# Kernel tuning notes

Hardware: AMD Instinct MI355X
Metric: run time of the kernel (lower is better)

Reference implementation:

```python
import jax, jax.numpy as jnp
import numpy as np

# ---- model hyperparameters (match init_kwargs) ----
D_MODEL = 1024
D_STATE = 128
EXPAND = 2
HEADDIM = 64
NGROUPS = 1
D_INNER = EXPAND * D_MODEL            # 2048
NHEADS = D_INNER // HEADDIM           # 32
ROPE_FRAC = 0.5
SPLIT = int(D_STATE * ROPE_FRAC)      # 64 rotary dims
NANG = SPLIT // 2                     # 32 rope angles
A_FLOOR = 1e-4
EPS = 1e-5
BATCH, SEQLEN = 1, 1024
SIZES = [D_INNER, D_INNER, D_STATE * NGROUPS, D_STATE * NGROUPS, NHEADS, NHEADS, NHEADS, NANG]
D_IN_PROJ = int(np.sum(SIZES))        # 4480


def setup_inputs() -> dict:
    key = jax.random.key(0)
    ks = jax.random.split(key, 6)
    u = jax.random.normal(ks[0], (BATCH, SEQLEN, D_MODEL), dtype=jnp.float32)
    W_in = jax.random.normal(ks[1], (D_MODEL, D_IN_PROJ), dtype=jnp.float32) * 0.02
    # dt_bias ~ log(dt) for dt in [1e-3, 0.1] -> around -4
    dt_bias = jax.random.normal(ks[2], (NHEADS,), dtype=jnp.float32) * 0.5 - 4.0
    B_bias = jnp.ones((NHEADS, D_STATE), jnp.float32) + 0.01 * jax.random.normal(ks[3], (NHEADS, D_STATE), dtype=jnp.float32)
    C_bias = jnp.ones((NHEADS, D_STATE), jnp.float32) + 0.01 * jax.random.normal(ks[4], (NHEADS, D_STATE), dtype=jnp.float32)
    Bn_w = jnp.ones((D_STATE,), jnp.float32)
    Cn_w = jnp.ones((D_STATE,), jnp.float32)
    D_param = jnp.ones((NHEADS,), jnp.float32)
    W_out = jax.random.normal(ks[5], (D_INNER, D_MODEL), dtype=jnp.float32) * 0.02
    return {"u": u, "W_in": W_in, "dt_bias": dt_bias, "B_bias": B_bias, "C_bias": C_bias,
            "Bn_w": Bn_w, "Cn_w": Cn_w, "D_param": D_param, "W_out": W_out}


def _rmsnorm(v, w):
    return v * jax.lax.rsqrt(jnp.mean(v * v, axis=-1, keepdims=True) + EPS) * w


def _forward(u, W_in, dt_bias, B_bias, C_bias, Bn_w, Cn_w, D_param, W_out):
    b, l, _ = u.shape
    proj = u @ W_in                                   # (b, l, d_in_proj)
    idx = np.cumsum(SIZES)[:-1]
    z, x, Bp, Cp, dd_dt, dd_A, trap_raw, ang = jnp.split(proj, idx, axis=-1)
    z = z.reshape(b, l, NHEADS, HEADDIM)
    x = x.reshape(b, l, NHEADS, HEADDIM)
    # A = clamp(-softplus(.), max=-A_floor);  dt = softplus(. + dt_bias)
    A = jnp.minimum(-jax.nn.softplus(dd_A), -A_FLOOR)          # (b,l,H)
    dt = jax.nn.softplus(dd_dt + dt_bias)                      # (b,l,H)
    a = jnp.exp(A * dt)                                        # decay per step
    lam = jax.nn.sigmoid(trap_raw)                             # trapezoid gate
    # RMSNorm on B/C (ngroups=1), then per-head additive bias
    Bn = _rmsnorm(Bp, Bn_w)                                    # (b,l,N)
    Cn = _rmsnorm(Cp, Cn_w)
    Bh = Bn[:, :, None, :] + B_bias                            # (b,l,H,N)
    Ch = Cn[:, :, None, :] + C_bias
    # data-dependent rotary: cumulative angle = cumsum(angles * dt)
    theta = jnp.cumsum(ang[:, :, None, :] * dt[..., None], axis=1)  # (b,l,H,NANG)
    cos, sin = jnp.cos(theta), jnp.sin(theta)

    def rope(v):
        d1, d2, rest = v[..., :NANG], v[..., NANG:SPLIT], v[..., SPLIT:]
        return jnp.concatenate([d1 * cos - d2 * sin, d1 * sin + d2 * cos, rest], axis=-1)

    Bh, Ch = rope(Bh), rope(Ch)

    tfirst = lambda v: jnp.moveaxis(v, 1, 0)
    inputs = (tfirst(Bh), tfirst(Ch), tfirst(x), tfirst(a), tfirst(dt), tfirst(lam))
    h0 = jnp.zeros((b, NHEADS, HEADDIM, D_STATE), jnp.float32)
    k0 = jnp.zeros((b, NHEADS, D_STATE), jnp.float32)
    v0 = jnp.zeros((b, NHEADS, HEADDIM), jnp.float32)

    def step(carry, inp):
        h, kp, vp = carry
        Bt, Ct, xt, at, dtt, lamt = inp
        # trapezoidal selective-scan update:
        # h_t = a_t h_{t-1} + dt_t (lam_t B_t x_t + (1-lam_t) a_t B_{t-1} x_{t-1})
        cur = jnp.einsum('bhp,bhn->bhpn', xt, Bt) * (dtt * lamt)[..., None, None]
        prv = jnp.einsum('bhp,bhn->bhpn', vp, kp) * (dtt * (1.0 - lamt) * at)[..., None, None]
        h = at[..., None, None] * h + cur + prv
        yt = jnp.einsum('bhn,bhpn->bhp', Ct, h)
        return (h, Bt, xt), yt

    _, y = jax.lax.scan(step, (h0, k0, v0), inputs)          # (l,b,H,P)
    y = jnp.moveaxis(y, 0, 1) + D_param[None, None, :, None] * x
    y = y * jax.nn.silu(z)                                    # gated output (no out-proj norm)
    return y.reshape(b, l, D_INNER) @ W_out


def reference(u, W_in, dt_bias, B_bias, C_bias, Bn_w, Cn_w, D_param, W_out):
    return _forward(u, W_in, dt_bias, B_bias, C_bias, Bn_w, Cn_w, D_param, W_out)
```

## Files before the change

### kernel.cpp

```cpp
#include <hip/hip_runtime.h>
#include <stdint.h>

#define SEQ     1024
#define DPROJ   4480

typedef __attribute__((ext_vector_type(8))) short short8;
typedef __attribute__((ext_vector_type(4))) float f4;

__device__ __forceinline__ short f2b(float f){
  union { float f; uint32_t u; } v; v.f = f;
  uint32_t r = (v.u + 0x7fffu + ((v.u >> 16) & 1u)) >> 16;
  return (short)(uint16_t)r;
}
__device__ __forceinline__ float b2f(uint16_t u){
  union { uint32_t u; float f; } v; v.u = ((uint32_t)u) << 16; return v.f;
}
__device__ __forceinline__ uint32_t pack2(float lo, float hi){
  return (uint32_t)(uint16_t)f2b(lo) | ((uint32_t)(uint16_t)f2b(hi) << 16);
}
__device__ __forceinline__ float softplus_f(float x){
  return x > 20.f ? x : log1pf(__expf(x));
}
__device__ __forceinline__ void gload_lds16(const short* g, short* l){
  __builtin_amdgcn_global_load_lds((const __attribute__((address_space(1))) void*)g,
                                   (__attribute__((address_space(3))) void*)l, 16, 0, 0);
}

__global__ __launch_bounds__(256) void cast_kernel(const float* __restrict__ in, short* __restrict__ out){
  int i = (blockIdx.x * 256 + threadIdx.x) * 4;
  f4 v = *(const f4*)(in + i);
  uint2 pk; pk.x = pack2(v.x, v.y); pk.y = pack2(v.z, v.w);
  *(uint2*)(out + i) = pk;
}

__global__ __launch_bounds__(256) void transpose_cast(const float* __restrict__ in, short* __restrict__ out,
                                                      int R, int C, int lda, int c0){
  __shared__ float tile[32][132];
  int bc = blockIdx.x * 32;
  int br = blockIdx.y * 128;
  int tid = threadIdx.x;
  int c = tid & 31, r0 = tid >> 5;
  #pragma unroll
  for (int i = 0; i < 16; i++){
    int r = r0 + i * 8;
    tile[c][r] = in[(size_t)(br + r) * lda + c0 + bc + c];
  }
  __syncthreads();
  #pragma unroll
  for (int i = 0; i < 4; i++){
    int task = tid + 256 * i;
    int cc = task >> 5;
    int rg = (task & 31) * 4;
    f4 v = *(const f4*)&tile[cc][rg];
    uint2 pk; pk.x = pack2(v.x, v.y); pk.y = pack2(v.z, v.w);
    *(uint2*)(out + (size_t)(bc + cc) * R + br + rg) = pk;
  }
}

__global__ __launch_bounds__(256) void gemm1_kernel(const short* __restrict__ A, const short* __restrict__ Bt,
                                                    float* __restrict__ C){
  const int M = 1024, N = 4480, K = 1024;
  __shared__ __align__(16) short As[128 * 32];
  __shared__ __align__(16) short Bs[160 * 32];
  const int tid  = threadIdx.x;
  const int wave = tid >> 6;
  const int lane = tid & 63;
  const int m0 = blockIdx.y * 128;
  const int n0 = blockIdx.x * 160;
  const int wm = (wave >> 1) * 64;
  const int wn = (wave & 1) * 80;
  const int quad = lane >> 4;
  const int r16  = lane & 15;

  f4 acc[4][5];
  #pragma unroll
  for (int i = 0; i < 4; i++)
    #pragma unroll
    for (int j = 0; j < 5; j++) acc[i][j] = (f4){0.f, 0.f, 0.f, 0.f};

  const int row0 = tid >> 2;
  const int kq   = tid & 3;
  const short* gA0 = A  + (size_t)(m0 + row0) * K + kq * 8;
  const short* gA1 = A  + (size_t)(m0 + row0 + 64) * K + kq * 8;
  const short* gB0 = Bt + (size_t)(n0 + row0) * K + kq * 8;
  const short* gB1 = Bt + (size_t)(n0 + row0 + 64) * K + kq * 8;
  const short* gB2 = Bt + (size_t)(n0 + row0 + 128) * K + kq * 8;
  short* lA0 = &As[(size_t)tid * 8];
  short* lA1 = &As[(size_t)(tid + 256) * 8];
  short* lB0 = &Bs[(size_t)tid * 8];
  short* lB1 = &Bs[(size_t)(tid + 256) * 8];
  short* lB2 = &Bs[(size_t)(tid + 512) * 8];

  for (int kt = 0; kt < 32; ++kt){
    const int ko = kt * 32;
    __syncthreads();
    gload_lds16(gA0 + ko, lA0);
    gload_lds16(gA1 + ko, lA1);
    gload_lds16(gB0 + ko, lB0);
    gload_lds16(gB1 + ko, lB1);
    if (tid < 128) gload_lds16(gB2 + ko, lB2);
    __syncthreads();
    short8 af[4], bf[5];
    #pragma unroll
    for (int i = 0; i < 4; i++)
      af[i] = *(const short8*)&As[(wm + i * 16 + r16) * 32 + quad * 8];
    #pragma unroll
    for (int j = 0; j < 5; j++)
      bf[j] = *(const short8*)&Bs[(wn + j * 16 + r16) * 32 + quad * 8];
    #pragma unroll
    for (int i = 0; i < 4; i++)
      #pragma unroll
      for (int j = 0; j < 5; j++)
        acc[i][j] = __builtin_amdgcn_mfma_f32_16x16x32_bf16(af[i], bf[j], acc[i][j], 0, 0, 0);
  }

  #pragma unroll
  for (int i = 0; i < 4; i++)
    #pragma unroll
    for (int j = 0; j < 5; j++)
      #pragma unroll
      for (int rr = 0; rr < 4; ++rr){
        int row = m0 + wm + i * 16 + quad * 4 + rr;
        int col = n0 + wn + j * 16 + r16;
        C[(size_t)row * N + col] = acc[i][j][rr];
      }
}

__global__ __launch_bounds__(256) void gemm2_kernel(const short* __restrict__ A, const short* __restrict__ Bt,
                                                    float* __restrict__ C){
  const int N = 1024, K = 2048, klen = 512;
  __shared__ __align__(16) short As[128 * 32];
  __shared__ __align__(16) short Bs[128 * 32];
  const int tid  = threadIdx.x;
  const int wave = tid >> 6;
  const int lane = tid & 63;
  const int m0 = blockIdx.y * 128;
  const int n0 = blockIdx.x * 128;
  const int k0 = blockIdx.z * klen;
  const int wm = (wave >> 1) * 64;
  const int wn = (wave & 1) * 64;
  const int quad = lane >> 4;
  const int r16  = lane & 15;

  f4 acc[4][4];
  #pragma unroll
  for (int i = 0; i < 4; i++)
    #pragma unroll
    for (int j = 0; j < 4; j++) acc[i][j] = (f4){0.f, 0.f, 0.f, 0.f};

  const int row0 = tid >> 2;
  const int kq   = tid & 3;
  const short* gA0 = A  + (size_t)(m0 + row0) * K + k0 + kq * 8;
  const short* gA1 = A  + (size_t)(m0 + row0 + 64) * K + k0 + kq * 8;
  const short* gB0 = Bt + (size_t)(n0 + row0) * K + k0 + kq * 8;
  const short* gB1 = Bt + (size_t)(n0 + row0 + 64) * K + k0 + kq * 8;
  short* lA0 = &As[(size_t)tid * 8];
  short* lA1 = &As[(size_t)(tid + 256) * 8];
  short* lB0 = &Bs[(size_t)tid * 8];
  short* lB1 = &Bs[(size_t)(tid + 256) * 8];

  for (int kt = 0; kt < klen / 32; ++kt){
    const int ko = kt * 32;
    __syncthreads();
    gload_lds16(gA0 + ko, lA0);
    gload_lds16(gA1 + ko, lA1);
    gload_lds16(gB0 + ko, lB0);
    gload_lds16(gB1 + ko, lB1);
    __syncthreads();
    short8 af[4], bf[4];
    #pragma unroll
    for (int i = 0; i < 4; i++){
      af[i] = *(const short8*)&As[(wm + i * 16 + r16) * 32 + quad * 8];
      bf[i] = *(const short8*)&Bs[(wn + i * 16 + r16) * 32 + quad * 8];
    }
    #pragma unroll
    for (int i = 0; i < 4; i++)
      #pragma unroll
      for (int j = 0; j < 4; j++)
        acc[i][j] = __builtin_amdgcn_mfma_f32_16x16x32_bf16(af[i], bf[j], acc[i][j], 0, 0, 0);
  }

  #pragma unroll
  for (int i = 0; i < 4; i++)
    #pragma unroll
    for (int j = 0; j < 4; j++)
      #pragma unroll
      for (int rr = 0; rr < 4; ++rr){
        int row = m0 + wm + i * 16 + quad * 4 + rr;
        int col = n0 + wn + j * 16 + r16;
        unsafeAtomicAdd(&C[(size_t)row * N + col], acc[i][j][rr]);
      }
}

__global__ __launch_bounds__(256) void scanL_kernel(const float* __restrict__ proj,
                                                    const float* __restrict__ dt_bias,
                                                    float* __restrict__ Lcum, float* __restrict__ u2b,
                                                    float* __restrict__ c1b, float* __restrict__ dtb){
  int h = blockIdx.x;
  int tid = threadIdx.x;
  int t0 = tid * 4;
  float dtbias = dt_bias[h];
  float dt5[5], lam5[5];
  #pragma unroll
  for (int i = 0; i < 5; i++){
    int t = t0 + i;
    if (t < 1024){
      const float* row = proj + (size_t)t * DPROJ;
      dt5[i]  = softplus_f(row[4352 + h] + dtbias);
      lam5[i] = 1.f / (1.f + __expf(-row[4416 + h]));
    } else { dt5[i] = 0.f; lam5[i] = 0.f; }
  }
  float v[4], c1[4], c2n[4];
  #pragma unroll
  for (int i = 0; i < 4; i++){
    int t = t0 + i;
    const float* row = proj + (size_t)t * DPROJ;
    float Ah = -fmaxf(softplus_f(row[4384 + h]), 1e-4f);
    v[i]   = Ah * dt5[i];
    c1[i]  = dt5[i] * lam5[i];
    c2n[i] = dt5[i + 1] * (1.f - lam5[i + 1]);
  }
  v[1] += v[0]; v[2] += v[1]; v[3] += v[2];
  float tot = v[3], sc = tot;
  int lane = tid & 63, wave = tid >> 6;
  #pragma unroll
  for (int off = 1; off < 64; off <<= 1){
    float n = __shfl_up(sc, off, 64);
    if (lane >= off) sc += n;
  }
  __shared__ float wsum[4];
  if (lane == 63) wsum[wave] = sc;
  __syncthreads();
  float base = sc - tot;
  for (int w = 0; w < wave; ++w) base += wsum[w];
  #pragma unroll
  for (int i = 0; i < 4; i++){
    int t = t0 + i;
    Lcum[h * 1024 + t] = base + v[i];
    u2b[h * 1024 + t]  = c1[i] + c2n[i];
    c1b[h * 1024 + t]  = c1[i];
    dtb[h * 1024 + t]  = dt5[i];
  }
}

__global__ __launch_bounds__(256) void theta2_kernel(const float* __restrict__ proj,
                                                     const float* __restrict__ dtb,
                                                     float* __restrict__ cosb, float* __restrict__ sinb){
  int h = blockIdx.x >> 5, k = blockIdx.x & 31;
  int tid = threadIdx.x;
  int t0 = tid * 4;
  f4 dtv = *(const f4*)&dtb[h * 1024 + t0];
  float v[4];
  #pragma unroll
  for (int i = 0; i < 4; i++)
    v[i] = proj[(size_t)(t0 + i) * DPROJ + 4448 + k] * dtv[i];
  v[1] += v[0]; v[2] += v[1]; v[3] += v[2];
  float tot = v[3], sc = tot;
  int lane = tid & 63, wave = tid >> 6;
  #pragma unroll
  for (int off = 1; off < 64; off <<= 1){
    float n = __shfl_up(sc, off, 64);
    if (lane >= off) sc += n;
  }
  __shared__ float wsum[4];
  if (lane == 63) wsum[wave] = sc;
  __syncthreads();
  float base = sc - tot;
  for (int w = 0; w < wave; ++w) base += wsum[w];
  #pragma unroll
  for (int i = 0; i < 4; i++){
    float th = base + v[i];
    float s, c;
    __sincosf(th, &s, &c);
    int t = t0 + i;
    cosb[(size_t)t * 1024 + h * 32 + k] = c;
    sinb[(size_t)t * 1024 + h * 32 + k] = s;
  }
}

__global__ __launch_bounds__(256) void bc_kernel(const float* __restrict__ proj,
                                                 const float* __restrict__ B_bias, const float* __restrict__ C_bias,
                                                 const float* __restrict__ Bn_w, const float* __restrict__ Cn_w,
                                                 const float* __restrict__ cosb, const float* __restrict__ sinb,
                                                 short* __restrict__ Bb, short* __restrict__ Cb){
  int t = blockIdx.x;
  int tid = threadIdx.x;
  __shared__ float vv[2][128];
  __shared__ float red[4];
  int n = tid & 127;
  int isC = tid >> 7;
  float val = proj[(size_t)t * DPROJ + 4096 + isC * 128 + n];
  float ss = val * val;
  #pragma unroll
  for (int off = 32; off >= 1; off >>= 1) ss += __shfl_down(ss, off);
  int wave = tid >> 6, lane = tid & 63;
  if (lane == 0) red[wave] = ss;
  __syncthreads();
  float rsv = isC ? rsqrtf((red[2] + red[3]) * (1.f / 128.f) + 1e-5f)
                  : rsqrtf((red[0] + red[1]) * (1.f / 128.f) + 1e-5f);
  vv[isC][n] = val * rsv * (isC ? Cn_w[n] : Bn_w[n]);
  __syncthreads();
  const float* cb = cosb + (size_t)t * 1024;
  const float* sb = sinb + (size_t)t * 1024;
  #pragma unroll
  for (int it = 0; it < 8; it++){
    int task = tid + 256 * it;
    int arr  = task >> 10;
    int rem  = task & 1023;
    int h    = rem >> 5;
    int n0   = (rem & 31) * 4;
    const float* bias = arr ? C_bias : B_bias;
    const float* base = vv[arr];
    f4 bv = *(const f4*)&base[n0];
    f4 bi = *(const f4*)&bias[h * 128 + n0];
    f4 o;
    if (n0 < 32){
      f4 bv2 = *(const f4*)&base[n0 + 32];
      f4 bi2 = *(const f4*)&bias[h * 128 + n0 + 32];
      f4 cv = *(const f4*)&cb[h * 32 + n0];
      f4 sv = *(const f4*)&sb[h * 32 + n0];
      #pragma unroll
      for (int q = 0; q < 4; q++) o[q] = (bv[q] + bi[q]) * cv[q] - (bv2[q] + bi2[q]) * sv[q];
    } else if (n0 < 64){
      int k0 = n0 - 32;
      f4 bv1 = *(const f4*)&base[k0];
      f4 bi1 = *(const f4*)&bias[h * 128 + k0];
      f4 cv = *(const f4*)&cb[h * 32 + k0];
      f4 sv = *(const f4*)&sb[h * 32 + k0];
      #pragma unroll
      for (int q = 0; q < 4; q++) o[q] = (bv1[q] + bi1[q]) * sv[q] + (bv[q] + bi[q]) * cv[q];
    } else {
      #pragma unroll
      for (int q = 0; q < 4; q++) o[q] = bv[q] + bi[q];
    }
    uint2 pk; pk.x = pack2(o.x, o.y); pk.y = pack2(o.z, o.w);
    short* outp = arr ? Cb : Bb;
    *(uint2*)(outp + (size_t)t * 4096 + h * 128 + n0) = pk;
  }
}

__global__ __launch_bounds__(256) void hpart_kernel(const short* __restrict__ xTb, const short* __restrict__ Bb,
                                                    const float* __restrict__ Lcum, const float* __restrict__ u2b,
                                                    short* __restrict__ Hpart){
  int h = blockIdx.x >> 3, c = blockIdx.x & 7;
  int t0 = c * 128;
  int tid = threadIdx.x;
  __shared__ float wS[128];
  if (tid < 128){
    float Lend = Lcum[h * 1024 + t0 + 127];
    wS[tid] = __expf(Lend - Lcum[h * 1024 + t0 + tid]) * u2b[h * 1024 + t0 + tid];
  }
  __syncthreads();
  int wave = tid >> 6, lane = tid & 63, quad = lane >> 4, r16 = lane & 15;
  int n0 = wave * 32;
  f4 acc[4][2];
  #pragma unroll
  for (int i = 0; i < 4; i++)
    #pragma unroll
    for (int j = 0; j < 2; j++) acc[i][j] = (f4){0.f, 0.f, 0.f, 0.f};

  const ushort* Bh = (const ushort*)Bb + (size_t)t0 * 4096 + h * 128;
  #pragma unroll
  for (int kk = 0; kk < 4; ++kk){
    int sb = kk * 32 + quad * 8;
    short8 af[4];
    #pragma unroll
    for (int i = 0; i < 4; i++){
      int p = i * 16 + r16;
      af[i] = *(const short8*)(xTb + (size_t)(h * 64 + p) * 1024 + t0 + sb);
    }
    float wv[8];
    #pragma unroll
    for (int jj = 0; jj < 8; jj++) wv[jj] = wS[sb + jj];
    short8 bfr[2];
    #pragma unroll
    for (int j = 0; j < 2; j++){
      int nn = n0 + j * 16 + r16;
      float e[8];
      #pragma unroll
      for (int jj = 0; jj < 8; jj++)
        e[jj] = b2f(Bh[(size_t)(sb + jj) * 4096 + nn]) * wv[jj];
      union { short8 s; uint32_t u[4]; } fr;
      #pragma unroll
      for (int q = 0; q < 4; q++) fr.u[q] = pack2(e[2 * q], e[2 * q + 1]);
      bfr[j] = fr.s;
    }
    #pragma unroll
    for (int i = 0; i < 4; i++)
      #pragma unroll
      for (int j = 0; j < 2; j++)
        acc[i][j] = __builtin_amdgcn_mfma_f32_16x16x32_bf16(af[i], bfr[j], acc[i][j], 0, 0, 0);
  }

  short* out = Hpart + ((size_t)(h * 8 + c)) * 8192;
  #pragma unroll
  for (int i = 0; i < 4; i++)
    #pragma unroll
    for (int rr = 0; rr < 4; ++rr){
      int p = i * 16 + quad * 4 + rr;
      #pragma unroll
      for (int j = 0; j < 2; j++){
        int nn = n0 + j * 16 + r16;
        out[p * 128 + nn] = f2b(acc[i][j][rr]);
      }
    }
}

__global__ __launch_bounds__(256) void hscan_kernel(const short* __restrict__ Hpart,
                                                    const float* __restrict__ Lcum,
                                                    short* __restrict__ Hused){
  int idx = blockIdx.x * 256 + threadIdx.x;
  int h = idx >> 13, rem = idx & 8191;
  float acc = 0.f;
  float Lprev = 0.f;
  #pragma unroll
  for (int c = 0; c < 8; c++){
    Hused[((size_t)(h * 8 + c)) * 8192 + rem] = f2b(acc);
    float Lend = Lcum[h * 1024 + c * 128 + 127];
    float dec = __expf(Lend - Lprev);
    acc = dec * acc + b2f((uint16_t)Hpart[((size_t)(h * 8 + c)) * 8192 + rem]);
    Lprev = Lend;
  }
}

#define GS 144
__global__ __launch_bounds__(256) void chunky_kernel(const short* __restrict__ Cb, const short* __restrict__ Bbg,
                                                     const short* __restrict__ xTb, const short* __restrict__ Hused,
                                                     const float* __restrict__ Lcum, const float* __restrict__ u2b,
                                                     const float* __restrict__ c1b,
                                                     const float* __restrict__ proj, const float* __restrict__ D_par,
                                                     short* __restrict__ yb16){
  int h = blockIdx.x >> 3, c = blockIdx.x & 7;
  int t0 = c * 128;
  __shared__ __align__(16) short Gt[128 * GS];
  __shared__ float Lc[128], u2v[128], c1v[128];
  int tid = threadIdx.x;
  if (tid < 128){
    Lc[tid]  = Lcum[h * 1024 + t0 + tid];
    u2v[tid] = u2b[h * 1024 + t0 + tid];
    c1v[tid] = c1b[h * 1024 + t0 + tid];
  }
  float Lprev = (c > 0) ? Lcum[h * 1024 + t0 - 1] : 0.f;
  float Dp = D_par[h];
  int wave = tid >> 6, lane = tid & 63, quad = lane >> 4, r16 = lane & 15;
  int wm = (wave >> 1) * 64, wn = (wave & 1) * 64;

  f4 acc[4][4];
  #pragma unroll
  for (int i = 0; i < 4; i++)
    #pragma unroll
    for (int j = 0; j < 4; j++) acc[i][j] = (f4){0.f, 0.f, 0.f, 0.f};
  #pragma unroll
  for (int kk = 0; kk < 4; ++kk){
    short8 af[4], bf[4];
    #pragma unroll
    for (int i = 0; i < 4; i++)
      af[i] = *(const short8*)(Cb + (size_t)(t0 + wm + i * 16 + r16) * 4096 + h * 128 + kk * 32 + quad * 8);
    #pragma unroll
    for (int j = 0; j < 4; j++)
      bf[j] = *(const short8*)(Bbg + (size_t)(t0 + wn + j * 16 + r16) * 4096 + h * 128 + kk * 32 + quad * 8);
    #pragma unroll
    for (int i = 0; i < 4; i++)
      #pragma unroll
      for (int j = 0; j < 4; j++)
        acc[i][j] = __builtin_amdgcn_mfma_f32_16x16x32_bf16(af[i], bf[j], acc[i][j], 0, 0, 0);
  }
  __syncthreads();

  #pragma unroll
  for (int i = 0; i < 4; i++){
    #pragma unroll
    for (int rr = 0; rr < 4; ++rr){
      int trow = wm + i * 16 + quad * 4 + rr;
      float Lt = Lc[trow];
      #pragma unroll
      for (int j = 0; j < 4; j++){
        int scol = wn + j * 16 + r16;
        float g = 0.f;
        if (scol <= trow){
          float wcoef = (scol == trow) ? c1v[scol] : u2v[scol];
          g = acc[i][j][rr] * wcoef * __expf(Lt - Lc[scol]);
        }
        Gt[trow * GS + scol] = f2b(g);
      }
    }
  }
  __syncthreads();

  f4 accY[2][4], accZ[2][4];
  #pragma unroll
  for (int i = 0; i < 2; i++)
    #pragma unroll
    for (int j = 0; j < 4; j++){ accY[i][j] = (f4){0.f,0.f,0.f,0.f}; accZ[i][j] = (f4){0.f,0.f,0.f,0.f}; }
  int m0 = wave * 32;
  #pragma unroll
  for (int kk = 0; kk < 4; ++kk){
    short8 ag[2], ac[2], bx[4], bh[4];
    #pragma unroll
    for (int i = 0; i < 2; i++){
      ag[i] = *(const short8*)&Gt[(m0 + i * 16 + r16) * GS + kk * 32 + quad * 8];
      ac[i] = *(const short8*)(Cb + (size_t)(t0 + m0 + i * 16 + r16) * 4096 + h * 128 + kk * 32 + quad * 8);
    }
    #pragma unroll
    for (int j = 0; j < 4; j++){
      bx[j] = *(const short8*)(xTb + (size_t)(h * 64 + j * 16 + r16) * 1024 + t0 + kk * 32 + quad * 8);
      bh[j] = *(const short8*)(Hused + ((size_t)(h * 8 + c) * 64 + j * 16 + r16) * 128 + kk * 32 + quad * 8);
    }
    #pragma unroll
    for (int i = 0; i < 2; i++)
      #pragma unroll
      for (int j = 0; j < 4; j++){
        accY[i][j] = __builtin_amdgcn_mfma_f32_16x16x32_bf16(ag[i], bx[j], accY[i][j], 0, 0, 0);
        accZ[i][j] = __builtin_amdgcn_mfma_f32_16x16x32_bf16(ac[i], bh[j], accZ[i][j], 0, 0, 0);
      }
  }
  #pragma unroll
  for (int i = 0; i < 2; i++)
    #pragma unroll
    for (int rr = 0; rr < 4; ++rr){
      int trow = m0 + i * 16 + quad * 4 + rr;
      float ei = __expf(Lc[trow] - Lprev);
      const float* prow = proj + (size_t)(t0 + trow) * DPROJ;
      #pragma unroll
      for (int j = 0; j < 4; j++){
        int col = h * 64 + j * 16 + r16;
        float zv = prow[col];
        float xv = prow[2048 + col];
        float yv = accY[i][j][rr] + ei * accZ[i][j][rr] + Dp * xv;
        float o = yv * (zv / (1.f + __expf(-zv)));
        yb16[(size_t)(t0 + trow) * 2048 + col] = f2b(o);
      }
    }
}

extern "C" void kernel_launch(void* const* d_in, const int* in_sizes, int n_in,
                              void* d_out, int out_size, void* d_ws, size_t ws_size,
                              hipStream_t stream){
  const float* u       = (const float*)d_in[0];
  const float* W_in    = (const float*)d_in[1];
  const float* dt_bias = (const float*)d_in[2];
  const float* B_bias  = (const float*)d_in[3];
  const float* C_bias  = (const float*)d_in[4];
  const float* Bn_w    = (const float*)d_in[5];
  const float* Cn_w    = (const float*)d_in[6];
  const float* D_par   = (const float*)d_in[7];
  const float* W_out   = (const float*)d_in[8];
  float* out = (float*)d_out;

  char* ws = (char*)d_ws;
  short* u16   = (short*)(ws + 0);
  short* WtIn  = (short*)(ws + 2097152);
  short* WtOut = (short*)(ws + 11272192);
  float* proj  = (float*)(ws + 15466496);
  float* cosb  = (float*)(ws + 33816576);
  float* sinb  = (float*)(ws + 38010880);
  short* Bb    = (short*)(ws + 42205184);
  short* Cb    = (short*)(ws + 50593792);
  short* xTb   = (short*)(ws + 58982400);
  float* Lcum  = (float*)(ws + 63176704);
  float* u2b   = (float*)(ws + 63307776);
  float* c1b   = (float*)(ws + 63438848);
  float* dtb   = (float*)(ws + 63569920);
  short* Hpart = (short*)(ws + 63700992);
  short* Hused = (short*)(ws + 67895296);
  short* yb16  = (short*)(ws + 72089600);

  hipMemsetAsync(out, 0, (size_t)out_size * sizeof(float), stream);
  cast_kernel<<<1024, 256, 0, stream>>>(u, u16);
  transpose_cast<<<dim3(140, 8), 256, 0, stream>>>(W_in, WtIn, 1024, 4480, 4480, 0);
  transpose_cast<<<dim3(32, 16), 256, 0, stream>>>(W_out, WtOut, 2048, 1024, 1024, 0);
  gemm1_kernel<<<dim3(28, 8), 256, 0, stream>>>(u16, WtIn, proj);
  scanL_kernel<<<32, 256, 0, stream>>>(proj, dt_bias, Lcum, u2b, c1b, dtb);
  theta2_kernel<<<1024, 256, 0, stream>>>(proj, dtb, cosb, sinb);
  bc_kernel<<<1024, 256, 0, stream>>>(proj, B_bias, C_bias, Bn_w, Cn_w, cosb, sinb, Bb, Cb);
  transpose_cast<<<dim3(64, 8), 256, 0, stream>>>(proj, xTb, 1024, 2048, 4480, 2048);
  hpart_kernel<<<256, 256, 0, stream>>>(xTb, Bb, Lcum, u2b, Hpart);
  hscan_kernel<<<1024, 256, 0, stream>>>(Hpart, Lcum, Hused);
  chunky_kernel<<<256, 256, 0, stream>>>(Cb, Bb, xTb, Hused, Lcum, u2b, c1b, proj, D_par, yb16);
  gemm2_kernel<<<dim3(8, 8, 4), 256, 0, stream>>>(yb16, WtOut, out);
}
```

Measured before the change: 218.9 us.

## Fuse prep, scan, and transpose launches; double-buffer GEMMs; fold hscan into chunky

Several ideas land together. The input casts, both weight transposes and the output zeroing now run as one kernel, and the scanL and theta kernels are merged, with theta recomputing dt itself. The xT transpose is folded into the B/C normalisation kernel, and the separate inter-chunk state scan is removed so each chunky block accumulates decayed partial states from Hpart into LDS. Both GEMMs get double-buffered LDS so the next tile's loads overlap compute. This cuts launch count and removes the Hused round trip, but adds redundant per-block Hpart accumulation work and doubles the GEMMs' LDS footprint.

```diff
diff --git a/kernel.cpp b/kernel.cpp
--- a/kernel.cpp
+++ b/kernel.cpp
@@ -26,24 +26,34 @@
                                    (__attribute__((address_space(3))) void*)l, 16, 0, 0);
 }
 
-__global__ __launch_bounds__(256) void cast_kernel(const float* __restrict__ in, short* __restrict__ out){
-  int i = (blockIdx.x * 256 + threadIdx.x) * 4;
-  f4 v = *(const f4*)(in + i);
-  uint2 pk; pk.x = pack2(v.x, v.y); pk.y = pack2(v.z, v.w);
-  *(uint2*)(out + i) = pk;
-}
-
-__global__ __launch_bounds__(256) void transpose_cast(const float* __restrict__ in, short* __restrict__ out,
-                                                      int R, int C, int lda, int c0){
+__global__ __launch_bounds__(256) void prep_inputs(const float* __restrict__ u, short* __restrict__ u16,
+                                                   const float* __restrict__ W_in, short* __restrict__ WtIn,
+                                                   const float* __restrict__ W_out, short* __restrict__ WtOut,
+                                                   float* __restrict__ outz){
+  int b = blockIdx.x;
+  int tid = threadIdx.x;
+  if (b < 1024){
+    int i = (b * 256 + tid) * 4;
+    f4 v = *(const f4*)(u + i);
+    uint2 pk; pk.x = pack2(v.x, v.y); pk.y = pack2(v.z, v.w);
+    *(uint2*)(u16 + i) = pk;
+    return;
+  }
+  if (b >= 2656){
+    int i = ((b - 2656) * 256 + tid) * 4;
+    *(f4*)(outz + i) = (f4){0.f, 0.f, 0.f, 0.f};
+    return;
+  }
+  const float* in; short* outp; int R, lda, bx, by;
+  if (b < 2144){ int idx = b - 1024; bx = idx % 140; by = idx / 140; in = W_in;  outp = WtIn;  R = 1024; lda = 4480; }
+  else         { int idx = b - 2144; bx = idx & 31;  by = idx >> 5;  in = W_out; outp = WtOut; R = 2048; lda = 1024; }
   __shared__ float tile[32][132];
-  int bc = blockIdx.x * 32;
-  int br = blockIdx.y * 128;
-  int tid = threadIdx.x;
+  int bc = bx * 32, br = by * 128;
   int c = tid & 31, r0 = tid >> 5;
   #pragma unroll
   for (int i = 0; i < 16; i++){
     int r = r0 + i * 8;
-    tile[c][r] = in[(size_t)(br + r) * lda + c0 + bc + c];
+    tile[c][r] = in[(size_t)(br + r) * lda + bc + c];
   }
   __syncthreads();
   #pragma unroll
@@ -53,15 +63,15 @@
     int rg = (task & 31) * 4;
     f4 v = *(const f4*)&tile[cc][rg];
     uint2 pk; pk.x = pack2(v.x, v.y); pk.y = pack2(v.z, v.w);
-    *(uint2*)(out + (size_t)(bc + cc) * R + br + rg) = pk;
+    *(uint2*)(outp + (size_t)(bc + cc) * R + br + rg) = pk;
   }
 }
 
 __global__ __launch_bounds__(256) void gemm1_kernel(const short* __restrict__ A, const short* __restrict__ Bt,
                                                     float* __restrict__ C){
-  const int M = 1024, N = 4480, K = 1024;
-  __shared__ __align__(16) short As[128 * 32];
-  __shared__ __align__(16) short Bs[160 * 32];
+  const int N = 4480, K = 1024;
+  __shared__ __align__(16) short As[2][128 * 32];
+  __shared__ __align__(16) short Bs[2][160 * 32];
   const int tid  = threadIdx.x;
   const int wave = tid >> 6;
   const int lane = tid & 63;
@@ -85,28 +95,32 @@
   const short* gB0 = Bt + (size_t)(n0 + row0) * K + kq * 8;
   const short* gB1 = Bt + (size_t)(n0 + row0 + 64) * K + kq * 8;
   const short* gB2 = Bt + (size_t)(n0 + row0 + 128) * K + kq * 8;
-  short* lA0 = &As[(size_t)tid * 8];
-  short* lA1 = &As[(size_t)(tid + 256) * 8];
-  short* lB0 = &Bs[(size_t)tid * 8];
-  short* lB1 = &Bs[(size_t)(tid + 256) * 8];
-  short* lB2 = &Bs[(size_t)(tid + 512) * 8];
+
+  gload_lds16(gA0, &As[0][(size_t)tid * 8]);
+  gload_lds16(gA1, &As[0][(size_t)(tid + 256) * 8]);
+  gload_lds16(gB0, &Bs[0][(size_t)tid * 8]);
+  gload_lds16(gB1, &Bs[0][(size_t)(tid + 256) * 8]);
+  if (tid < 128) gload_lds16(gB2, &Bs[0][(size_t)(tid + 512) * 8]);
 
   for (int kt = 0; kt < 32; ++kt){
-    const int ko = kt * 32;
+    const int cur = kt & 1;
     __syncthreads();
-    gload_lds16(gA0 + ko, lA0);
-    gload_lds16(gA1 + ko, lA1);
-    gload_lds16(gB0 + ko, lB0);
-    gload_lds16(gB1 + ko, lB1);
-    if (tid < 128) gload_lds16(gB2 + ko, lB2);
-    __syncthreads();
+    if (kt + 1 < 32){
+      const int ko = (kt + 1) * 32;
+      const int nxt = cur ^ 1;
+      gload_lds16(gA0 + ko, &As[nxt][(size_t)tid * 8]);
+      gload_lds16(gA1 + ko, &As[nxt][(size_t)(tid + 256) * 8]);
+      gload_lds16(gB0 + ko, &Bs[nxt][(size_t)tid * 8]);
+      gload_lds16(gB1 + ko, &Bs[nxt][(size_t)(tid + 256) * 8]);
+      if (tid < 128) gload_lds16(gB2 + ko, &Bs[nxt][(size_t)(tid + 512) * 8]);
+    }
     short8 af[4], bf[5];
     #pragma unroll
     for (int i = 0; i < 4; i++)
-      af[i] = *(const short8*)&As[(wm + i * 16 + r16) * 32 + quad * 8];
+      af[i] = *(const short8*)&As[cur][(wm + i * 16 + r16) * 32 + quad * 8];
     #pragma unroll
     for (int j = 0; j < 5; j++)
-      bf[j] = *(const short8*)&Bs[(wn + j * 16 + r16) * 32 + quad * 8];
+      bf[j] = *(const short8*)&Bs[cur][(wn + j * 16 + r16) * 32 + quad * 8];
     #pragma unroll
     for (int i = 0; i < 4; i++)
       #pragma unroll
@@ -129,8 +143,8 @@
 __global__ __launch_bounds__(256) void gemm2_kernel(const short* __restrict__ A, const short* __restrict__ Bt,
                                                     float* __restrict__ C){
   const int N = 1024, K = 2048, klen = 512;
-  __shared__ __align__(16) short As[128 * 32];
-  __shared__ __align__(16) short Bs[128 * 32];
+  __shared__ __align__(16) short As[2][128 * 32];
+  __shared__ __align__(16) short Bs[2][128 * 32];
   const int tid  = threadIdx.x;
   const int wave = tid >> 6;
   const int lane = tid & 63;
@@ -154,24 +168,28 @@
   const short* gA1 = A  + (size_t)(m0 + row0 + 64) * K + k0 + kq * 8;
   const short* gB0 = Bt + (size_t)(n0 + row0) * K + k0 + kq * 8;
   const short* gB1 = Bt + (size_t)(n0 + row0 + 64) * K + k0 + kq * 8;
-  short* lA0 = &As[(size_t)tid * 8];
-  short* lA1 = &As[(size_t)(tid + 256) * 8];
-  short* lB0 = &Bs[(size_t)tid * 8];
-  short* lB1 = &Bs[(size_t)(tid + 256) * 8];
+
+  gload_lds16(gA0, &As[0][(size_t)tid * 8]);
+  gload_lds16(gA1, &As[0][(size_t)(tid + 256) * 8]);
+  gload_lds16(gB0, &Bs[0][(size_t)tid * 8]);
+  gload_lds16(gB1, &Bs[0][(size_t)(tid + 256) * 8]);
 
   for (int kt = 0; kt < klen / 32; ++kt){
-    const int ko = kt * 32;
+    const int cur = kt & 1;
     __syncthreads();
-    gload_lds16(gA0 + ko, lA0);
-    gload_lds16(gA1 + ko, lA1);
-    gload_lds16(gB0 + ko, lB0);
-    gload_lds16(gB1 + ko, lB1);
-    __syncthreads();
+    if (kt + 1 < klen / 32){
+      const int ko = (kt + 1) * 32;
+      const int nxt = cur ^ 1;
+      gload_lds16(gA0 + ko, &As[nxt][(size_t)tid * 8]);
+      gload_lds16(gA1 + ko, &As[nxt][(size_t)(tid + 256) * 8]);
+      gload_lds16(gB0 + ko, &Bs[nxt][(size_t)tid * 8]);
+      gload_lds16(gB1 + ko, &Bs[nxt][(size_t)(tid + 256) * 8]);
+    }
     short8 af[4], bf[4];
     #pragma unroll
     for (int i = 0; i < 4; i++){
-      af[i] = *(const short8*)&As[(wm + i * 16 + r16) * 32 + quad * 8];
-      bf[i] = *(const short8*)&Bs[(wn + i * 16 + r16) * 32 + quad * 8];
+      af[i] = *(const short8*)&As[cur][(wm + i * 16 + r16) * 32 + quad * 8];
+      bf[i] = *(const short8*)&Bs[cur][(wn + i * 16 + r16) * 32 + quad * 8];
     }
     #pragma unroll
     for (int i = 0; i < 4; i++)
@@ -192,99 +210,123 @@
       }
 }
 
-__global__ __launch_bounds__(256) void scanL_kernel(const float* __restrict__ proj,
-                                                    const float* __restrict__ dt_bias,
-                                                    float* __restrict__ Lcum, float* __restrict__ u2b,
-                                                    float* __restrict__ c1b, float* __restrict__ dtb){
-  int h = blockIdx.x;
+__global__ __launch_bounds__(256) void scan_theta(const float* __restrict__ proj,
+                                                  const float* __restrict__ dt_bias,
+                                                  float* __restrict__ Lcum, float* __restrict__ u2b,
+                                                  float* __restrict__ c1b,
+                                                  float* __restrict__ cosb, float* __restrict__ sinb){
+  int b = blockIdx.x;
   int tid = threadIdx.x;
   int t0 = tid * 4;
-  float dtbias = dt_bias[h];
-  float dt5[5], lam5[5];
-  #pragma unroll
-  for (int i = 0; i < 5; i++){
-    int t = t0 + i;
-    if (t < 1024){
+  int lane = tid & 63, wave = tid >> 6;
+  __shared__ float wsum[4];
+  if (b < 32){
+    int h = b;
+    float dtbias = dt_bias[h];
+    float dt5[5], lam5[5];
+    #pragma unroll
+    for (int i = 0; i < 5; i++){
+      int t = t0 + i;
+      if (t < 1024){
+        const float* row = proj + (size_t)t * DPROJ;
+        dt5[i]  = softplus_f(row[4352 + h] + dtbias);
+        lam5[i] = 1.f / (1.f + __expf(-row[4416 + h]));
+      } else { dt5[i] = 0.f; lam5[i] = 0.f; }
+    }
+    float v[4], c1[4], c2n[4];
+    #pragma unroll
+    for (int i = 0; i < 4; i++){
+      int t = t0 + i;
       const float* row = proj + (size_t)t * DPROJ;
-      dt5[i]  = softplus_f(row[4352 + h] + dtbias);
-      lam5[i] = 1.f / (1.f + __expf(-row[4416 + h]));
-    } else { dt5[i] = 0.f; lam5[i] = 0.f; }
-  }
-  float v[4], c1[4], c2n[4];
-  #pragma unroll
-  for (int i = 0; i < 4; i++){
-    int t = t0 + i;
-    const float* row = proj + (size_t)t * DPROJ;
-    float Ah = -fmaxf(softplus_f(row[4384 + h]), 1e-4f);
-    v[i]   = Ah * dt5[i];
-    c1[i]  = dt5[i] * lam5[i];
-    c2n[i] = dt5[i + 1] * (1.f - lam5[i + 1]);
-  }
-  v[1] += v[0]; v[2] += v[1]; v[3] += v[2];
-  float tot = v[3], sc = tot;
-  int lane = tid & 63, wave = tid >> 6;
-  #pragma unroll
-  for (int off = 1; off < 64; off <<= 1){
-    float n = __shfl_up(sc, off, 64);
-    if (lane >= off) sc += n;
-  }
-  __shared__ float wsum[4];
-  if (lane == 63) wsum[wave] = sc;
-  __syncthreads();
-  float base = sc - tot;
-  for (int w = 0; w < wave; ++w) base += wsum[w];
-  #pragma unroll
-  for (int i = 0; i < 4; i++){
-    int t = t0 + i;
-    Lcum[h * 1024 + t] = base + v[i];
-    u2b[h * 1024 + t]  = c1[i] + c2n[i];
-    c1b[h * 1024 + t]  = c1[i];
-    dtb[h * 1024 + t]  = dt5[i];
-  }
-}
-
-__global__ __launch_bounds__(256) void theta2_kernel(const float* __restrict__ proj,
-                                                     const float* __restrict__ dtb,
-                                                     float* __restrict__ cosb, float* __restrict__ sinb){
-  int h = blockIdx.x >> 5, k = blockIdx.x & 31;
+      float Ah = -fmaxf(softplus_f(row[4384 + h]), 1e-4f);
+      v[i]   = Ah * dt5[i];
+      c1[i]  = dt5[i] * lam5[i];
+      c2n[i] = dt5[i + 1] * (1.f - lam5[i + 1]);
+    }
+    v[1] += v[0]; v[2] += v[1]; v[3] += v[2];
+    float tot = v[3], sc = tot;
+    #pragma unroll
+    for (int off = 1; off < 64; off <<= 1){
+      float n = __shfl_up(sc, off, 64);
+      if (lane >= off) sc += n;
+    }
+    if (lane == 63) wsum[wave] = sc;
+    __syncthreads();
+    float base = sc - tot;
+    for (int w = 0; w < wave; ++w) base += wsum[w];
+    #pragma unroll
+    for (int i = 0; i < 4; i++){
+      int t = t0 + i;
+      Lcum[h * 1024 + t] = base + v[i];
+      u2b[h * 1024 + t]  = c1[i] + c2n[i];
+      c1b[h * 1024 + t]  = c1[i];
+    }
+  } else {
+    int hk = b - 32;
+    int h = hk >> 5, k = hk & 31;
+    float dtbias = dt_bias[h];
+    float v[4];
+    #pragma unroll
+    for (int i = 0; i < 4; i++){
+      const float* row = proj + (size_t)(t0 + i) * DPROJ;
+      float dt = softplus_f(row[4352 + h] + dtbias);
+      v[i] = row[4448 + k] * dt;
+    }
+    v[1] += v[0]; v[2] += v[1]; v[3] += v[2];
+    float tot = v[3], sc = tot;
+    #pragma unroll
+    for (int off = 1; off < 64; off <<= 1){
+      float n = __shfl_up(sc, off, 64);
+      if (lane >= off) sc += n;
+    }
+    if (lane == 63) wsum[wave] = sc;
+    __syncthreads();
+    float base = sc - tot;
+    for (int w = 0; w < wave; ++w) base += wsum[w];
+    #pragma unroll
+    for (int i = 0; i < 4; i++){
+      float th = base + v[i];
+      float s, c;
+      __sincosf(th, &s, &c);
+      int t = t0 + i;
+      cosb[(size_t)t * 1024 + h * 32 + k] = c;
+      sinb[(size_t)t * 1024 + h * 32 + k] = s;
+    }
+  }
+}
+
+__global__ __launch_bounds__(256) void bcxt_kernel(const float* __restrict__ proj,
+                                                   const float* __restrict__ B_bias, const float* __restrict__ C_bias,
+                                                   const float* __restrict__ Bn_w, const float* __restrict__ Cn_w,
+                                                   const float* __restrict__ cosb, const float* __restrict__ sinb,
+                                                   short* __restrict__ Bb, short* __restrict__ Cb,
+                                                   short* __restrict__ xTb){
+  int b = blockIdx.x;
   int tid = threadIdx.x;
-  int t0 = tid * 4;
-  f4 dtv = *(const f4*)&dtb[h * 1024 + t0];
-  float v[4];
-  #pragma unroll
-  for (int i = 0; i < 4; i++)
-    v[i] = proj[(size_t)(t0 + i) * DPROJ + 4448 + k] * dtv[i];
-  v[1] += v[0]; v[2] += v[1]; v[3] += v[2];
-  float tot = v[3], sc = tot;
-  int lane = tid & 63, wave = tid >> 6;
-  #pragma unroll
-  for (int off = 1; off < 64; off <<= 1){
-    float n = __shfl_up(sc, off, 64);
-    if (lane >= off) sc += n;
-  }
-  __shared__ float wsum[4];
-  if (lane == 63) wsum[wave] = sc;
-  __syncthreads();
-  float base = sc - tot;
-  for (int w = 0; w < wave; ++w) base += wsum[w];
-  #pragma unroll
-  for (int i = 0; i < 4; i++){
-    float th = base + v[i];
-    float s, c;
-    __sincosf(th, &s, &c);
-    int t = t0 + i;
-    cosb[(size_t)t * 1024 + h * 32 + k] = c;
-    sinb[(size_t)t * 1024 + h * 32 + k] = s;
-  }
-}
-
-__global__ __launch_bounds__(256) void bc_kernel(const float* __restrict__ proj,
-                                                 const float* __restrict__ B_bias, const float* __restrict__ C_bias,
-                                                 const float* __restrict__ Bn_w, const float* __restrict__ Cn_w,
-                                                 const float* __restrict__ cosb, const float* __restrict__ sinb,
-                                                 short* __restrict__ Bb, short* __restrict__ Cb){
-  int t = blockIdx.x;
-  int tid = threadIdx.x;
+  if (b >= 1024){
+    int idx = b - 1024;
+    int bx = idx & 63, by = idx >> 6;
+    __shared__ float tile[32][132];
+    int bc = bx * 32, br = by * 128;
+    int c = tid & 31, r0 = tid >> 5;
+    #pragma unroll
+    for (int i = 0; i < 16; i++){
+      int r = r0 + i * 8;
+      tile[c][r] = proj[(size_t)(br + r) * 4480 + 2048 + bc + c];
+    }
+    __syncthreads();
+    #pragma unroll
+    for (int i = 0; i < 4; i++){
+      int task = tid + 256 * i;
+      int cc = task >> 5;
+      int rg = (task & 31) * 4;
+      f4 v = *(const f4*)&tile[cc][rg];
+      uint2 pk; pk.x = pack2(v.x, v.y); pk.y = pack2(v.z, v.w);
+      *(uint2*)(xTb + (size_t)(bc + cc) * 1024 + br + rg) = pk;
+    }
+    return;
+  }
+  int t = b;
   __shared__ float vv[2][128];
   __shared__ float red[4];
   int n = tid & 127;
@@ -406,26 +448,10 @@
     }
 }
 
-__global__ __launch_bounds__(256) void hscan_kernel(const short* __restrict__ Hpart,
-                                                    const float* __restrict__ Lcum,
-                                                    short* __restrict__ Hused){
-  int idx = blockIdx.x * 256 + threadIdx.x;
-  int h = idx >> 13, rem = idx & 8191;
-  float acc = 0.f;
-  float Lprev = 0.f;
-  #pragma unroll
-  for (int c = 0; c < 8; c++){
-    Hused[((size_t)(h * 8 + c)) * 8192 + rem] = f2b(acc);
-    float Lend = Lcum[h * 1024 + c * 128 + 127];
-    float dec = __expf(Lend - Lprev);
-    acc = dec * acc + b2f((uint16_t)Hpart[((size_t)(h * 8 + c)) * 8192 + rem]);
-    Lprev = Lend;
-  }
-}
-
 #define GS 144
+#define HS 136
 __global__ __launch_bounds__(256) void chunky_kernel(const short* __restrict__ Cb, const short* __restrict__ Bbg,
-                                                     const short* __restrict__ xTb, const short* __restrict__ Hused,
+                                                     const short* __restrict__ xTb, const short* __restrict__ Hpart,
                                                      const float* __restrict__ Lcum, const float* __restrict__ u2b,
                                                      const float* __restrict__ c1b,
                                                      const float* __restrict__ proj, const float* __restrict__ D_par,
@@ -433,6 +459,7 @@
   int h = blockIdx.x >> 3, c = blockIdx.x & 7;
   int t0 = c * 128;
   __shared__ __align__(16) short Gt[128 * GS];
+  __shared__ __align__(16) short Hacc[64 * HS];
   __shared__ float Lc[128], u2v[128], c1v[128];
   int tid = threadIdx.x;
   if (tid < 128){
@@ -444,6 +471,23 @@
   float Dp = D_par[h];
   int wave = tid >> 6, lane = tid & 63, quad = lane >> 4, r16 = lane & 15;
   int wm = (wave >> 1) * 64, wn = (wave & 1) * 64;
+
+  float scs[7];
+  #pragma unroll
+  for (int cp = 0; cp < 7; cp++)
+    scs[cp] = (cp < c) ? __expf(Lprev - Lcum[h * 1024 + cp * 128 + 127]) : 0.f;
+  #pragma unroll
+  for (int i = 0; i < 16; i++){
+    int e2 = tid + 256 * i;
+    float a0 = 0.f, a1 = 0.f;
+    for (int cp = 0; cp < c; cp++){
+      uint32_t pr = *(const uint32_t*)(Hpart + ((size_t)(h * 8 + cp)) * 8192 + (size_t)e2 * 2);
+      a0 += b2f((uint16_t)(pr & 0xffffu)) * scs[cp];
+      a1 += b2f((uint16_t)(pr >> 16)) * scs[cp];
+    }
+    int p = e2 >> 6, n2 = e2 & 63;
+    *(uint32_t*)&Hacc[p * HS + n2 * 2] = pack2(a0, a1);
+  }
 
   f4 acc[4][4];
   #pragma unroll
@@ -504,7 +548,7 @@
     #pragma unroll
     for (int j = 0; j < 4; j++){
       bx[j] = *(const short8*)(xTb + (size_t)(h * 64 + j * 16 + r16) * 1024 + t0 + kk * 32 + quad * 8);
-      bh[j] = *(const short8*)(Hused + ((size_t)(h * 8 + c) * 64 + j * 16 + r16) * 128 + kk * 32 + quad * 8);
+      bh[j] = *(const short8*)&Hacc[(j * 16 + r16) * HS + kk * 32 + quad * 8];
     }
     #pragma unroll
     for (int i = 0; i < 2; i++)
@@ -560,22 +604,14 @@
   float* Lcum  = (float*)(ws + 63176704);
   float* u2b   = (float*)(ws + 63307776);
   float* c1b   = (float*)(ws + 63438848);
-  float* dtb   = (float*)(ws + 63569920);
-  short* Hpart = (short*)(ws + 63700992);
-  short* Hused = (short*)(ws + 67895296);
-  short* yb16  = (short*)(ws + 72089600);
-
-  hipMemsetAsync(out, 0, (size_t)out_size * sizeof(float), stream);
-  cast_kernel<<<1024, 256, 0, stream>>>(u, u16);
-  transpose_cast<<<dim3(140, 8), 256, 0, stream>>>(W_in, WtIn, 1024, 4480, 4480, 0);
-  transpose_cast<<<dim3(32, 16), 256, 0, stream>>>(W_out, WtOut, 2048, 1024, 1024, 0);
+  short* Hpart = (short*)(ws + 63569920);
+  short* yb16  = (short*)(ws + 67764224);
+
+  prep_inputs<<<3680, 256, 0, stream>>>(u, u16, W_in, WtIn, W_out, WtOut, out);
   gemm1_kernel<<<dim3(28, 8), 256, 0, stream>>>(u16, WtIn, proj);
-  scanL_kernel<<<32, 256, 0, stream>>>(proj, dt_bias, Lcum, u2b, c1b, dtb);
-  theta2_kernel<<<1024, 256, 0, stream>>>(proj, dtb, cosb, sinb);
-  bc_kernel<<<1024, 256, 0, stream>>>(proj, B_bias, C_bias, Bn_w, Cn_w, cosb, sinb, Bb, Cb);
-  transpose_cast<<<dim3(64, 8), 256, 0, stream>>>(proj, xTb, 1024, 2048, 4480, 2048);
+  scan_theta<<<1056, 256, 0, stream>>>(proj, dt_bias, Lcum, u2b, c1b, cosb, sinb);
+  bcxt_kernel<<<1536, 256, 0, stream>>>(proj, B_bias, C_bias, Bn_w, Cn_w, cosb, sinb, Bb, Cb, xTb);
   hpart_kernel<<<256, 256, 0, stream>>>(xTb, Bb, Lcum, u2b, Hpart);
-  hscan_kernel<<<1024, 256, 0, stream>>>(Hpart, Lcum, Hused);
-  chunky_kernel<<<256, 256, 0, stream>>>(Cb, Bb, xTb, Hused, Lcum, u2b, c1b, proj, D_par, yb16);
+  chunky_kernel<<<256, 256, 0, stream>>>(Cb, Bb, xTb, Hpart, Lcum, u2b, c1b, proj, D_par, yb16);
   gemm2_kernel<<<dim3(8, 8, 4), 256, 0, stream>>>(yb16, WtOut, out);
 }
```

Measured after the change: 242.9 us. 1.11x slower.
